# Kernel tuning notes

Hardware: AMD Instinct MI355X
Metric: run time of the kernel (lower is better)

Reference implementation:

```python
import jax, jax.numpy as jnp
import numpy as np

H = 256        # hidden_dim
GD = 16        # genome_dim
GL = 16        # genome_len
L = 2          # n_layers
NH = 4         # n_heads
ED = 256       # embed_dim (of generated network)
CS = 256       # chunk_size (== H so chunk feedback into GRU is well-formed)
TOTAL = 4 * ED * ED + 4 * ED          # 263168
NCH = (TOTAL + CS - 1) // CS          # 1028 sequential GRU steps
B = 16


def setup_inputs() -> dict:
    key = jax.random.key(0)
    ks = iter(jax.random.split(key, 32))
    def p(shape, s=0.02):
        return jax.random.normal(next(ks), shape, jnp.float32) * s
    return dict(
        genome_seq=jax.random.normal(next(ks), (B, GL, GD), jnp.float32),
        embed_W=p((H, GD)), embed_b=jnp.zeros((H,), jnp.float32),
        qkv_W=p((L, 3 * H, H)), qkv_b=jnp.zeros((L, 3 * H), jnp.float32),
        attn_out_W=p((L, H, H)), attn_out_b=jnp.zeros((L, H), jnp.float32),
        ln1_g=jnp.ones((L, H), jnp.float32), ln1_b=jnp.zeros((L, H), jnp.float32),
        ln2_g=jnp.ones((L, H), jnp.float32), ln2_b=jnp.zeros((L, H), jnp.float32),
        ffn_W1=p((L, 4 * H, H)), ffn_b1=jnp.zeros((L, 4 * H), jnp.float32),
        ffn_W2=p((L, H, 4 * H)), ffn_b2=jnp.zeros((L, H), jnp.float32),
        gru_Wih=p((3 * H, H)), gru_Whh=p((3 * H, H)),
        gru_bih=jnp.zeros((3 * H,), jnp.float32), gru_bhh=jnp.zeros((3 * H,), jnp.float32),
        out_W=p((CS, H)), out_b=jnp.zeros((CS,), jnp.float32),
    )


def _ln(x, g, b, eps=1e-5):
    m = x.mean(-1, keepdims=True)
    v = ((x - m) ** 2).mean(-1, keepdims=True)
    return (x - m) / jnp.sqrt(v + eps) * g + b


def reference(genome_seq, embed_W, embed_b, qkv_W, qkv_b, attn_out_W, attn_out_b,
              ln1_g, ln1_b, ln2_g, ln2_b, ffn_W1, ffn_b1, ffn_W2, ffn_b2,
              gru_Wih, gru_Whh, gru_bih, gru_bhh, out_W, out_b):
    b = genome_seq.shape[0]
    dh = H // NH
    scale = 1.0 / np.sqrt(dh).astype(np.float32)

    h = genome_seq @ embed_W.T + embed_b                      # [B, S, H]
    # post-norm transformer encoder, relu FFN (PyTorch defaults, no dropout)
    for l in range(L):
        qkv = h @ qkv_W[l].T + qkv_b[l]                        # [B, S, 3H]
        q, k, v = jnp.split(qkv, 3, axis=-1)
        q = q.reshape(b, GL, NH, dh)
        k = k.reshape(b, GL, NH, dh)
        v = v.reshape(b, GL, NH, dh)
        scores = jnp.einsum('bshd,bthd->bhst', q, k) * scale
        attn = jax.nn.softmax(scores, axis=-1)
        o = jnp.einsum('bhst,bthd->bshd', attn, v).reshape(b, GL, H)
        h = _ln(h + o @ attn_out_W[l].T + attn_out_b[l], ln1_g[l], ln1_b[l])
        f = jax.nn.relu(h @ ffn_W1[l].T + ffn_b1[l]) @ ffn_W2[l].T + ffn_b2[l]
        h = _ln(h + f, ln2_g[l], ln2_b[l])

    latent = h.mean(axis=1)                                    # [B, H]

    # sequential chunk generation: 1 GRU step + Linear per chunk, fed back
    def step(carry, _):
        x, hid = carry
        gi = x @ gru_Wih.T + gru_bih
        gh = hid @ gru_Whh.T + gru_bhh
        ir, iz, inn = jnp.split(gi, 3, axis=-1)
        hr, hz, hn = jnp.split(gh, 3, axis=-1)
        r = jax.nn.sigmoid(ir + hr)
        z = jax.nn.sigmoid(iz + hz)
        n = jnp.tanh(inn + r * hn)
        hid = (1.0 - z) * n + z * hid
        chunk = hid @ out_W.T + out_b                          # [B, CS]
        return (chunk, hid), chunk

    h0 = jnp.zeros((b, H), latent.dtype)
    _, chunks = jax.lax.scan(step, (latent, h0), None, length=NCH)  # [NCH, B, CS]
    flat = jnp.moveaxis(chunks, 0, 1).reshape(b, NCH * CS)
    return flat[:, :TOTAL]
```

## Files before the change

kernel.cpp:

```cpp
#include <hip/hip_runtime.h>


typedef unsigned int uint_t;
typedef int v4i __attribute__((ext_vector_type(4)));

static constexpr size_t WS_HB   = 0;
static constexpr size_t WS_AO   = 262144;
static constexpr size_t WS_CV   = 606208;
static constexpr size_t WS_MS   = 607232;
static constexpr size_t WS_M8   = 608256;
static constexpr size_t WS_HSEQ = 673792;

__device__ inline float sigf(float x){
    return __builtin_amdgcn_rcpf(1.0f + __builtin_amdgcn_exp2f(-1.442695041f*x));
}
__device__ inline float tanh_fast(float x){
    return 1.0f - 2.0f*__builtin_amdgcn_rcpf(1.0f + __builtin_amdgcn_exp2f(2.885390082f*x));
}


__global__ __launch_bounds__(256) void k_pre(
    const float* gs, const float* eW, const float* eb,
    const float* qkvW, const float* qkvb,
    const float* Wih, const float* Whh, const float* bih, const float* bhh,
    const float* outW, const float* outb, float* ws)
{
    __shared__ float s_h[16][256];
    __shared__ float s_qkv[3][16][64];
    __shared__ float s_sc[16][16];

    int tid = threadIdx.x;

    if(blockIdx.x >= 64){
        __shared__ float wrow[256]; __shared__ float red[256];
        __shared__ signed char q8[256];
        int r = blockIdx.x - 64, c = tid;
        bool hasA = (r<768);
        wrow[c] = hasA ? Wih[(size_t)r*256+c] : 0.0f;
        __syncthreads();
        float m;
        if(hasA){
            float a=0.f;
            for(int k=0;k<256;++k) a += wrow[k]*outW[(size_t)k*256+c];
            if(r<512) a += Whh[(size_t)r*256+c];
            m=a;
        } else {
            m = Whh[(size_t)(r-256)*256+c];
        }
        red[c] = wrow[c]*outb[c];
        __syncthreads();
        for(int off=128;off>0;off>>=1){ if(c<off) red[c]+=red[c+off]; __syncthreads(); }
        if(c==0){
            float cv;
            if(r<512)       cv = red[0] + bih[r] + bhh[r];
            else if(r<768)  cv = red[0] + bih[r];
            else            cv = bhh[r-256];
            ws[WS_CV + r] = cv;
        }
        __syncthreads();
        red[c] = fabsf(m);
        __syncthreads();
        for(int off=128;off>0;off>>=1){ if(c<off) red[c]=fmaxf(red[c],red[c+off]); __syncthreads(); }
        float rowmax = red[0];
        float inv = rowmax>0.f ? 127.0f/rowmax : 0.0f;
        q8[c] = (signed char)__float2int_rn(m*inv);
        if(c==0) ws[WS_MS + r] = rowmax>0.f ? rowmax*(1.0f/(127.0f*127.0f)) : 0.0f;
        __syncthreads();
        if(c<64){
            uint_t u = ((uint_t)(unsigned char)q8[4*c  ])
                     | ((uint_t)(unsigned char)q8[4*c+1] << 8)
                     | ((uint_t)(unsigned char)q8[4*c+2] << 16)
                     | ((uint_t)(unsigned char)q8[4*c+3] << 24);
            ((uint_t*)ws)[WS_M8 + (size_t)r*64 + c] = u;
        }
        return;
    }

    int b = blockIdx.x>>2, hh = blockIdx.x&3;

    {
        int i = tid;
        float ew[16];
#pragma unroll
        for(int d=0;d<16;++d) ew[d] = eW[i*16+d];
        float bias = eb[i];
#pragma unroll
        for(int s=0;s<16;++s){
            const float* g = gs + (b*16+s)*16;
            float acc = bias;
#pragma unroll
            for(int d=0;d<16;++d) acc += g[d]*ew[d];
            s_h[s][i] = acc;
            if(hh==0) ws[WS_HB + (size_t)(b*16+s)*256 + i] = acc;
        }
    }
    __syncthreads();

    if(tid<192){
        int p = tid>>6, d = tid&63;
        int row = p*256 + hh*64 + d;
        const float* wr = qkvW + (size_t)row*256;
        float bias = qkvb[row];
        float acc[16];
#pragma unroll
        for(int s=0;s<16;++s) acc[s]=bias;
        for(int k=0;k<256;k+=4){
            float4 w4 = *(const float4*)(wr+k);
#pragma unroll
            for(int s=0;s<16;++s){
                float4 h4 = *(const float4*)&s_h[s][k];
                acc[s] += w4.x*h4.x + w4.y*h4.y + w4.z*h4.z + w4.w*h4.w;
            }
        }
#pragma unroll
        for(int s=0;s<16;++s) s_qkv[p][s][d] = acc[s];
    }
    __syncthreads();
    {
        int s = tid>>4, t = tid&15;
        float a=0.f;
#pragma unroll
        for(int d=0; d<64; ++d) a += s_qkv[0][s][d]*s_qkv[1][t][d];
        s_sc[s][t] = a*0.125f;
    }
    __syncthreads();
    if(tid<16){
        int r=tid;
        float m=-1e30f;
#pragma unroll
        for(int tt=0;tt<16;++tt) m=fmaxf(m,s_sc[r][tt]);
        float e[16]; float sum=0.f;
#pragma unroll
        for(int tt=0;tt<16;++tt){ e[tt]=__expf(s_sc[r][tt]-m); sum+=e[tt]; }
        float inv=1.0f/sum;
#pragma unroll
        for(int tt=0;tt<16;++tt) s_sc[r][tt]=e[tt]*inv;
    }
    __syncthreads();
    for(int u=tid; u<1024; u+=256){
        int s=u>>6, d=u&63;
        float o=0.f;
#pragma unroll
        for(int t2=0;t2<16;++t2) o += s_sc[s][t2]*s_qkv[2][t2][d];
        ws[WS_AO + (size_t)(b*16+s)*256 + hh*64 + d] = o;
    }
}


__global__ __launch_bounds__(256) void k_qkv_attn(const float* qkvW, const float* qkvb,
                                                  float* ws, int l){
    __shared__ float s_h[16][256];
    __shared__ float s_q[16][64], s_k[16][64], s_v[16][64];
    __shared__ float s_sc[16][16];
    int b = blockIdx.x>>2, hh = blockIdx.x&3;
    int tid = threadIdx.x;

    for(int u=tid; u<4096; u+=256)
        s_h[u>>8][u&255] = ws[WS_HB + (size_t)(b*16+(u>>8))*256 + (u&255)];
    __syncthreads();

    if(tid<192){
        int p = tid>>6, d = tid&63;
        int row = l*768 + p*256 + hh*64 + d;
        const float* wr = qkvW + (size_t)row*256;
        float bias = qkvb[row];
        float acc[16];
#pragma unroll
        for(int s=0;s<16;++s) acc[s]=bias;
        for(int k=0;k<256;k+=4){
            float4 w4 = *(const float4*)(wr+k);
#pragma unroll
            for(int s=0;s<16;++s){
                float4 h4 = *(const float4*)&s_h[s][k];
                acc[s] += w4.x*h4.x + w4.y*h4.y + w4.z*h4.z + w4.w*h4.w;
            }
        }
        float (*dst)[64] = (p==0) ? s_q : (p==1) ? s_k : s_v;
#pragma unroll
        for(int s=0;s<16;++s) dst[s][d] = acc[s];
    }
    __syncthreads();
    {
        int s = tid>>4, t = tid&15;
        float a=0.f;
#pragma unroll
        for(int d=0; d<64; ++d) a += s_q[s][d]*s_k[t][d];
        s_sc[s][t] = a*0.125f;
    }
    __syncthreads();
    if(tid<16){
        int r=tid;
        float m=-1e30f;
#pragma unroll
        for(int tt=0;tt<16;++tt) m=fmaxf(m,s_sc[r][tt]);
        float e[16]; float sum=0.f;
#pragma unroll
        for(int tt=0;tt<16;++tt){ e[tt]=__expf(s_sc[r][tt]-m); sum+=e[tt]; }
        float inv=1.0f/sum;
#pragma unroll
        for(int tt=0;tt<16;++tt) s_sc[r][tt]=e[tt]*inv;
    }
    __syncthreads();
    for(int u=tid; u<1024; u+=256){
        int s=u>>6, d=u&63;
        float o=0.f;
#pragma unroll
        for(int t2=0;t2<16;++t2) o += s_sc[s][t2]*s_v[t2][d];
        ws[WS_AO + (size_t)(b*16+s)*256 + hh*64 + d] = o;
    }
}


__global__ __launch_bounds__(256) void k_ao_ffn(
    const float* aoW, const float* aob, const float* g1, const float* b1,
    const float* W1, const float* fb1, const float* W2, const float* fb2,
    const float* g2, const float* b2v, float* ws, int l)
{
    __shared__ float s_x[256];
    __shared__ float s_f1[1024];
    __shared__ float red[256];
    int bs = blockIdx.x, i = threadIdx.x;

    s_x[i] = ws[WS_AO + (size_t)bs*256 + i];
    float hb = ws[WS_HB + (size_t)bs*256 + i];
    __syncthreads();

    const float* wr = aoW + (size_t)(l*256+i)*256;
    float acc = aob[l*256+i];
    for(int k=0;k<256;k+=4){
        float4 w4 = *(const float4*)(wr+k);
        float4 h4 = *(const float4*)&s_x[k];
        acc += w4.x*h4.x + w4.y*h4.y + w4.z*h4.z + w4.w*h4.w;
    }
    float x = hb + acc;
    red[i]=x; __syncthreads();
    for(int off=128;off>0;off>>=1){ if(i<off) red[i]+=red[i+off]; __syncthreads(); }
    float mn = red[0]*(1.0f/256.0f); __syncthreads();
    float d = x-mn;
    red[i]=d*d; __syncthreads();
    for(int off=128;off>0;off>>=1){ if(i<off) red[i]+=red[i+off]; __syncthreads(); }
    float vv = red[0]*(1.0f/256.0f);
    float h1 = (d / sqrtf(vv+1e-5f))*g1[l*256+i] + b1[l*256+i];
    __syncthreads();
    s_x[i] = h1;
    __syncthreads();

#pragma unroll
    for(int jj=0;jj<4;++jj){
        int j = jj*256 + i;
        const float* w1r = W1 + (size_t)(l*1024+j)*256;
        float a1 = fb1[l*1024+j];
        for(int k=0;k<256;k+=4){
            float4 w4 = *(const float4*)(w1r+k);
            float4 h4 = *(const float4*)&s_x[k];
            a1 += w4.x*h4.x + w4.y*h4.y + w4.z*h4.z + w4.w*h4.w;
        }
        s_f1[j] = fmaxf(a1, 0.0f);
    }
    __syncthreads();

    const float* w2r = W2 + (size_t)(l*256+i)*1024;
    float a2 = fb2[l*256+i];
    for(int k=0;k<1024;k+=4){
        float4 w4 = *(const float4*)(w2r+k);
        float4 h4 = *(const float4*)&s_f1[k];
        a2 += w4.x*h4.x + w4.y*h4.y + w4.z*h4.z + w4.w*h4.w;
    }
    float x2 = h1 + a2;
    red[i]=x2; __syncthreads();
    for(int off=128;off>0;off>>=1){ if(i<off) red[i]+=red[i+off]; __syncthreads(); }
    float mn2 = red[0]*(1.0f/256.0f); __syncthreads();
    float d2 = x2-mn2;
    red[i]=d2*d2; __syncthreads();
    for(int off=128;off>0;off>>=1){ if(i<off) red[i]+=red[i+off]; __syncthreads(); }
    float vv2 = red[0]*(1.0f/256.0f);
    float y2 = d2 / sqrtf(vv2+1e-5f);
    ws[WS_HB + (size_t)bs*256 + i] = y2*g2[l*256+i] + b2v[l*256+i];
}


__global__ __launch_bounds__(512,2) void k_chain(const float* Wih, const float* bih,
                                                 const float* bhh, float* ws){
    __shared__ alignas(16) signed char h8[2][256];
    __shared__ float latl[256];
    __shared__ float gi0l[768];
    int tid = threadIdx.x;
    int b   = blockIdx.x;
    int l   = tid & 63;
    int w   = tid >> 6;
    int col = l & 15;
    int grp = l >> 4;
    int par = grp & 1;
    int ge  = w*32 + par*16 + col;

    if(tid<256){
        float a=0.f;
#pragma unroll
        for(int s=0;s<16;++s) a += ws[WS_HB + (size_t)(b*16+s)*256 + tid];
        latl[tid] = a*(1.0f/16.0f);
    }
    __syncthreads();
    for(int j=tid; j<768; j+=512){
        const float* wr = Wih + (size_t)j*256;
        float a = bih[j];
        for(int k=0;k<256;k+=4){
            float4 w4=*(const float4*)(wr+k);
            float4 l4=*(const float4*)&latl[k];
            a += w4.x*l4.x + w4.y*l4.y + w4.z*l4.z + w4.w*l4.w;
        }
        gi0l[j] = a;
    }
    __syncthreads();

    const uint_t* Mdw = (const uint_t*)ws + WS_M8;
    v4i wf[8][4];
#pragma unroll
    for(int s=0;s<4;++s){
#pragma unroll
        for(int half=0; half<2; ++half){
            int f = s*2 + half;
            int row = s*256 + w*32 + half*16 + col;
            const uint_t* src = Mdw + (size_t)row*64 + grp*4;
#pragma unroll
            for(int kt=0;kt<4;++kt)
                wf[f][kt] = *(const v4i*)(src + kt*16);
        }
    }
    float Cs[4], MSs[4];
#pragma unroll
    for(int s=0;s<4;++s){
        int row = s*256 + ge;
        Cs[s]  = ws[WS_CV + row];
        MSs[s] = ws[WS_MS + row];
    }

    float r0 = sigf(gi0l[ge]     + bhh[ge]);
    float z0 = sigf(gi0l[256+ge] + bhh[256+ge]);
    float n0 = tanh_fast(gi0l[512+ge] + r0*bhh[512+ge]);
    float hp = (1.0f-z0)*n0;

    float* hsp = ws + WS_HSEQ + (size_t)b*256;
    if(grp < 2){
        h8[0][w*32 + (l&31)] = (signed char)__float2int_rn(hp*127.0f);
        hsp[w*32 + (l&31)] = hp;
    }
    asm volatile("s_waitcnt lgkmcnt(0)" ::: "memory");
    __builtin_amdgcn_s_barrier();
    asm volatile("" ::: "memory");

    const v4i vzero = {0,0,0,0};
    int po = 0;
    for(int t=1; t<1028; ++t){
        hsp += 4096;
        v4i af[4];
#pragma unroll
        for(int kt=0;kt<4;++kt)
            af[kt] = *(const v4i*)&h8[po][kt*64 + grp*16];
        v4i acc[8];
#pragma unroll
        for(int f=0;f<8;++f){
            acc[f] = __builtin_amdgcn_mfma_i32_16x16x64_i8(af[0], wf[f][0], vzero, 0,0,0);
#pragma unroll
            for(int kt=1;kt<4;++kt)
                acc[f] = __builtin_amdgcn_mfma_i32_16x16x64_i8(af[kt], wf[f][kt], acc[f], 0,0,0);
        }
        int a_r = par ? acc[1][0] : acc[0][0];
        int a_z = par ? acc[3][0] : acc[2][0];
        int a_n = par ? acc[5][0] : acc[4][0];
        int a_h = par ? acc[7][0] : acc[6][0];
        float yr = MSs[0]*(float)a_r + Cs[0];
        float yz = MSs[1]*(float)a_z + Cs[1];
        float yn = MSs[2]*(float)a_n + Cs[2];
        float yh = MSs[3]*(float)a_h + Cs[3];
        float rr = sigf(yr);
        float zz = sigf(yz);
        float nn = tanh_fast(yn + rr*yh);
        hp = (1.0f-zz)*nn + zz*hp;
        if(grp < 2){
            h8[po^1][w*32 + (l&31)] = (signed char)__float2int_rn(hp*127.0f);
            hsp[w*32 + (l&31)] = hp;
        }
        asm volatile("s_waitcnt lgkmcnt(0)" ::: "memory");
        __builtin_amdgcn_s_barrier();
        asm volatile("" ::: "memory");
        po ^= 1;
    }
}


__global__ __launch_bounds__(256) void k_epi(const float* outW, const float* outb,
                                             const float* ws, float* out){
    __shared__ float ht[16][256];
    int t = blockIdx.x, j = threadIdx.x;
    for(int idx=j; idx<4096; idx+=256)
        ht[idx>>8][idx&255] = ws[WS_HSEQ + (size_t)t*4096 + idx];
    __syncthreads();
    const float* wr = outW + (size_t)j*256;
    float bias = outb[j];
    float acc[16];
#pragma unroll
    for(int bb=0;bb<16;++bb) acc[bb]=bias;
    for(int k=0;k<256;k+=4){
        float4 w4 = *(const float4*)(wr+k);
#pragma unroll
        for(int bb=0;bb<16;++bb)
            acc[bb] += w4.x*ht[bb][k]+w4.y*ht[bb][k+1]+w4.z*ht[bb][k+2]+w4.w*ht[bb][k+3];
    }
#pragma unroll
    for(int bb=0;bb<16;++bb)
        out[(size_t)bb*263168 + (size_t)t*256 + j] = acc[bb];
}


extern "C" void kernel_launch(void* const* d_in, const int* in_sizes, int n_in,
                              void* d_out, int out_size, void* d_ws, size_t ws_size,
                              hipStream_t stream){
    const float* gs   = (const float*)d_in[0];
    const float* eW   = (const float*)d_in[1];
    const float* eb   = (const float*)d_in[2];
    const float* qkvW = (const float*)d_in[3];
    const float* qkvb = (const float*)d_in[4];
    const float* aoW  = (const float*)d_in[5];
    const float* aob  = (const float*)d_in[6];
    const float* g1   = (const float*)d_in[7];
    const float* b1   = (const float*)d_in[8];
    const float* g2   = (const float*)d_in[9];
    const float* b2   = (const float*)d_in[10];
    const float* W1   = (const float*)d_in[11];
    const float* fb1  = (const float*)d_in[12];
    const float* W2   = (const float*)d_in[13];
    const float* fb2  = (const float*)d_in[14];
    const float* Wih  = (const float*)d_in[15];
    const float* Whh  = (const float*)d_in[16];
    const float* bih  = (const float*)d_in[17];
    const float* bhh  = (const float*)d_in[18];
    const float* outW = (const float*)d_in[19];
    const float* outb = (const float*)d_in[20];
    float* ws  = (float*)d_ws;
    float* out = (float*)d_out;

    k_pre     <<<1088,256,0,stream>>>(gs,eW,eb,qkvW,qkvb,Wih,Whh,bih,bhh,outW,outb,ws);
    k_ao_ffn  <<<256,256,0,stream>>>(aoW,aob,g1,b1,W1,fb1,W2,fb2,g2,b2,ws,0);
    k_qkv_attn<<<64,256,0,stream>>>(qkvW,qkvb,ws,1);
    k_ao_ffn  <<<256,256,0,stream>>>(aoW,aob,g1,b1,W1,fb1,W2,fb2,g2,b2,ws,1);
    k_chain   <<<16,512,0,stream>>>(Wih,bih,bhh,ws);
    k_epi     <<<1028,256,0,stream>>>(outW,outb,ws,out);
}
```

Measured before the change: 1.088 ms.

## Fuse final layer attn-out/FFN into GRU chain kernel prologue

Removes the separate layer-1 attention-output + FFN kernel launch and computes it inside k_chain, with each of the 16 blocks processing its own batch's 16 tokens two at a time and keeping results in shared memory for the latent mean. This saves a launch and a global round trip. In exchange, the work moves from 256 blocks to 16 blocks running sequentially over 8 iterations, each streaming the full FFN weights. Launch bounds also drop the 2-blocks-per-CU hint, and shared memory use grows a lot.

```diff
diff --git a/kernel.cpp b/kernel.cpp
--- a/kernel.cpp
+++ b/kernel.cpp
@@ -279,24 +279,84 @@
 }
 
 
-__global__ __launch_bounds__(512,2) void k_chain(const float* Wih, const float* bih,
-                                                 const float* bhh, float* ws){
+__global__ __launch_bounds__(512) void k_chain(
+    const float* aoW, const float* aob, const float* g1, const float* b1,
+    const float* W1, const float* fb1, const float* W2, const float* fb2,
+    const float* g2, const float* b2v,
+    const float* Wih, const float* bih, const float* bhh, float* ws)
+{
     __shared__ alignas(16) signed char h8[2][256];
+    __shared__ float s_hf[16][256];
+    __shared__ float s_f1[2][1024];
+    __shared__ float s_hx[2][256];
+    __shared__ float s_red[2][256];
     __shared__ float latl[256];
     __shared__ float gi0l[768];
     int tid = threadIdx.x;
     int b   = blockIdx.x;
-    int l   = tid & 63;
-    int w   = tid >> 6;
-    int col = l & 15;
-    int grp = l >> 4;
-    int par = grp & 1;
-    int ge  = w*32 + par*16 + col;
+
+    for(int it=0; it<8; ++it){
+        int tk = tid>>8, i = tid&255, s = it*2+tk;
+        int bs = b*16 + s;
+        s_hx[tk][i] = ws[WS_AO + (size_t)bs*256 + i];
+        float hb = ws[WS_HB + (size_t)bs*256 + i];
+        __syncthreads();
+        const float* wr = aoW + (size_t)(1*256+i)*256;
+        float acc = aob[1*256+i];
+        for(int k=0;k<256;k+=4){
+            float4 w4 = *(const float4*)(wr+k);
+            float4 a4 = *(const float4*)&s_hx[tk][k];
+            acc += w4.x*a4.x + w4.y*a4.y + w4.z*a4.z + w4.w*a4.w;
+        }
+        float x = hb + acc;
+        s_red[tk][i]=x; __syncthreads();
+        for(int off=128;off>0;off>>=1){ if(i<off) s_red[tk][i]+=s_red[tk][i+off]; __syncthreads(); }
+        float mn = s_red[tk][0]*(1.0f/256.0f); __syncthreads();
+        float d = x-mn;
+        s_red[tk][i]=d*d; __syncthreads();
+        for(int off=128;off>0;off>>=1){ if(i<off) s_red[tk][i]+=s_red[tk][i+off]; __syncthreads(); }
+        float vv = s_red[tk][0]*(1.0f/256.0f);
+        float h1 = (d / sqrtf(vv+1e-5f))*g1[1*256+i] + b1[1*256+i];
+        __syncthreads();
+        s_hx[tk][i] = h1;
+        __syncthreads();
+#pragma unroll
+        for(int jj=0;jj<4;++jj){
+            int j = jj*256 + i;
+            const float* w1r = W1 + (size_t)(1*1024+j)*256;
+            float a1 = fb1[1*1024+j];
+            for(int k=0;k<256;k+=4){
+                float4 w4 = *(const float4*)(w1r+k);
+                float4 h4 = *(const float4*)&s_hx[tk][k];
+                a1 += w4.x*h4.x + w4.y*h4.y + w4.z*h4.z + w4.w*h4.w;
+            }
+            s_f1[tk][j] = fmaxf(a1, 0.0f);
+        }
+        __syncthreads();
+        const float* w2r = W2 + (size_t)(1*256+i)*1024;
+        float a2 = fb2[1*256+i];
+        for(int k=0;k<1024;k+=4){
+            float4 w4 = *(const float4*)(w2r+k);
+            float4 h4 = *(const float4*)&s_f1[tk][k];
+            a2 += w4.x*h4.x + w4.y*h4.y + w4.z*h4.z + w4.w*h4.w;
+        }
+        float x2 = h1 + a2;
+        s_red[tk][i]=x2; __syncthreads();
+        for(int off=128;off>0;off>>=1){ if(i<off) s_red[tk][i]+=s_red[tk][i+off]; __syncthreads(); }
+        float mn2 = s_red[tk][0]*(1.0f/256.0f); __syncthreads();
+        float d2 = x2-mn2;
+        s_red[tk][i]=d2*d2; __syncthreads();
+        for(int off=128;off>0;off>>=1){ if(i<off) s_red[tk][i]+=s_red[tk][i+off]; __syncthreads(); }
+        float vv2 = s_red[tk][0]*(1.0f/256.0f);
+        float y2 = d2 / sqrtf(vv2+1e-5f);
+        s_hf[s][i] = y2*g2[1*256+i] + b2v[1*256+i];
+        __syncthreads();
+    }
 
     if(tid<256){
         float a=0.f;
 #pragma unroll
-        for(int s=0;s<16;++s) a += ws[WS_HB + (size_t)(b*16+s)*256 + tid];
+        for(int s=0;s<16;++s) a += s_hf[s][tid];
         latl[tid] = a*(1.0f/16.0f);
     }
     __syncthreads();
@@ -311,6 +371,15 @@
         gi0l[j] = a;
     }
     __syncthreads();
+
+    asm volatile("" ::: "memory");
+
+    int l   = tid & 63;
+    int w   = tid >> 6;
+    int col = l & 15;
+    int grp = l >> 4;
+    int par = grp & 1;
+    int ge  = w*32 + par*16 + col;
 
     const uint_t* Mdw = (const uint_t*)ws + WS_M8;
     v4i wf[8][4];
@@ -442,7 +511,6 @@
     k_pre     <<<1088,256,0,stream>>>(gs,eW,eb,qkvW,qkvb,Wih,Whh,bih,bhh,outW,outb,ws);
     k_ao_ffn  <<<256,256,0,stream>>>(aoW,aob,g1,b1,W1,fb1,W2,fb2,g2,b2,ws,0);
     k_qkv_attn<<<64,256,0,stream>>>(qkvW,qkvb,ws,1);
-    k_ao_ffn  <<<256,256,0,stream>>>(aoW,aob,g1,b1,W1,fb1,W2,fb2,g2,b2,ws,1);
-    k_chain   <<<16,512,0,stream>>>(Wih,bih,bhh,ws);
+    k_chain   <<<16,512,0,stream>>>(aoW,aob,g1,b1,W1,fb1,W2,fb2,g2,b2,Wih,bih,bhh,ws);
     k_epi     <<<1028,256,0,stream>>>(outW,outb,ws,out);
 }
```

After: 2.680 ms. 2.46x slower.
